# Kernel optimization log

Hardware: AMD Instinct MI355X
Metric: run time of the kernel (lower is better)

The kernel has to match this reference:

```python
import jax, jax.numpy as jnp
import numpy as np

N, C_IN, C_OUT, HID, H = 4096, 512, 512, 128, 4
HEAD_OUT = C_OUT // H  # 128
MID = 4 * C_OUT        # 2048
R = 1.0                # spatial radius r
L = 48                 # sequence window l
NEG = -1e9


def layer_norm(x, g, b, eps=1e-5):
    m = jnp.mean(x, axis=-1, keepdims=True)
    v = jnp.mean(jnp.square(x - m), axis=-1, keepdims=True)
    return (x - m) * jax.lax.rsqrt(v + eps) * g + b


def setup_inputs() -> dict:
    key = jax.random.key(0)
    ks = jax.random.split(key, 16)
    s = lambda fan: 1.0 / np.sqrt(fan)
    return {
        "x":   jax.random.normal(ks[0], (N, C_IN), jnp.float32),
        "pos": jax.random.normal(ks[1], (N, 3), jnp.float32),
        "ori": jax.random.normal(ks[2], (N, 3), jnp.float32),
        "seq": jnp.arange(N, dtype=jnp.int64) if jax.config.jax_enable_x64 else jnp.arange(N, dtype=jnp.int32),
        "batch": jnp.sort(jax.random.randint(ks[3], (N,), 0, 8)),
        "ln1_g": jnp.ones((C_IN,), jnp.float32),
        "ln1_b": jnp.zeros((C_IN,), jnp.float32),
        "ln2_g": jnp.ones((C_OUT,), jnp.float32),
        "ln2_b": jnp.zeros((C_OUT,), jnp.float32),
        "Wq": jax.random.normal(ks[4], (H, C_IN, HID), jnp.float32) * s(C_IN),
        "Wk": jax.random.normal(ks[5], (H, C_IN, HID), jnp.float32) * s(C_IN),
        "Wv": jax.random.normal(ks[6], (H, C_IN, HID), jnp.float32) * s(C_IN),
        "Wo": jax.random.normal(ks[7], (H, HID, HEAD_OUT), jnp.float32) * s(HID),
        "lnm_g": jnp.ones((MID,), jnp.float32),
        "lnm_b": jnp.zeros((MID,), jnp.float32),
        "W1": jax.random.normal(ks[8], (C_OUT, MID), jnp.float32) * s(C_OUT),
        "W2": jax.random.normal(ks[9], (MID, C_OUT), jnp.float32) * s(MID),
    }


def _block(x, pos, ori, seq, batch, ln1_g, ln1_b, ln2_g, ln2_b,
           Wq, Wk, Wv, Wo, lnm_g, lnm_b, W1, W2):
    identity = x
    xn = layer_norm(x, ln1_g, ln1_b)

    # geometry/sequence neighborhood mask: same graph, ||dp||<=r, |ds|<=l
    d2 = jnp.sum(jnp.square(pos[:, None, :] - pos[None, :, :]), axis=-1)  # [N,N]
    ds = jnp.abs(seq[:, None] - seq[None, :])
    mask = (batch[:, None] == batch[None, :]) & (d2 <= R * R) & (ds <= L)

    # all heads at once (original loops over heads; math identical)
    q = jnp.einsum('nc,hcd->hnd', xn, Wq)
    k = jnp.einsum('nc,hcd->hnd', xn, Wk)
    v = jnp.einsum('nc,hcd->hnd', xn, Wv)
    gbias = ori @ ori.T  # geometric orientation bias [N,N]
    scores = jnp.einsum('hnd,hmd->hnm', q, k) / np.sqrt(HID) + gbias[None]
    scores = jnp.where(mask[None], scores, NEG)
    attn = jax.nn.softmax(scores, axis=-1)
    o = jnp.einsum('hnm,hmd->hnd', attn, v)
    o = jnp.einsum('hnd,hde->hne', o, Wo)               # [H,N,HEAD_OUT]
    o = jnp.transpose(o, (1, 0, 2)).reshape(N, C_OUT)   # concat heads

    x = o + identity
    identity = x
    h = layer_norm(x, ln2_g, ln2_b) @ W1
    h = jax.nn.relu(layer_norm(h, lnm_g, lnm_b))
    return h @ W2 + identity


def reference(x, pos, ori, seq, batch, ln1_g, ln1_b, ln2_g, ln2_b,
              Wq, Wk, Wv, Wo, lnm_g, lnm_b, W1, W2):
    return _block(x, pos, ori, seq, batch, ln1_g, ln1_b, ln2_g, ln2_b,
                  Wq, Wk, Wv, Wo, lnm_g, lnm_b, W1, W2)
```

## Files before the change

kernel.cpp:

```cpp
#include <hip/hip_runtime.h>

typedef unsigned short u16;
typedef unsigned int u32;
typedef float f32x4 __attribute__((ext_vector_type(4)));
typedef __bf16 bf16x8 __attribute__((ext_vector_type(8)));

#define N_TOK 4096
#define QKV_LD 1536
#define NH 4
#define HID 128
#define C_OUT 512

__device__ __forceinline__ float b2f(u16 u) { return __uint_as_float(((u32)u) << 16); }
__device__ __forceinline__ u16 f2b(float f) {
  u32 u = __float_as_uint(f);
  u32 r = (u + 0x7fffu + ((u >> 16) & 1u)) >> 16;
  return (u16)r;
}

__global__ __launch_bounds__(256) void transpose_tile(
    const float* __restrict__ src, u16* __restrict__ dst, int R, int C)
{
  __shared__ u16 tile[32][33];
  const int b = blockIdx.z;
  const int c0 = blockIdx.x * 32, r0 = blockIdx.y * 32;
  const int tx = threadIdx.x & 31, ty = threadIdx.x >> 5;
  const float* s = src + (size_t)b * R * C;
  u16* d = dst + (size_t)b * R * C;
#pragma unroll
  for (int i = 0; i < 32; i += 8)
    tile[ty + i][tx] = f2b(s[(size_t)(r0 + ty + i) * C + c0 + tx]);
  __syncthreads();
#pragma unroll
  for (int i = 0; i < 32; i += 8)
    d[(size_t)(c0 + ty + i) * R + r0 + tx] = tile[tx][ty + i];
}

__global__ __launch_bounds__(256) void transpose_qkv(
    const float* __restrict__ Wq, const float* __restrict__ Wk,
    const float* __restrict__ Wv, u16* __restrict__ dst)
{
  __shared__ u16 tile[32][33];
  const int z = blockIdx.z;
  const int which = z >> 2, b = z & 3;
  const float* src = (which == 0) ? Wq : (which == 1) ? Wk : Wv;
  const int R = 512, C = 128;
  const int c0 = blockIdx.x * 32, r0 = blockIdx.y * 32;
  const int tx = threadIdx.x & 31, ty = threadIdx.x >> 5;
  const float* s = src + (size_t)b * R * C;
  u16* d = dst + (size_t)which * 4 * R * C + (size_t)b * R * C;
#pragma unroll
  for (int i = 0; i < 32; i += 8)
    tile[ty + i][tx] = f2b(s[(size_t)(r0 + ty + i) * C + c0 + tx]);
  __syncthreads();
#pragma unroll
  for (int i = 0; i < 32; i += 8)
    d[(size_t)(c0 + ty + i) * R + r0 + tx] = tile[tx][ty + i];
}

__global__ __launch_bounds__(256) void ln_kernel(
    const void* __restrict__ x, const float* __restrict__ g,
    const float* __restrict__ b, u16* __restrict__ y,
    int C, int in_f32, int do_relu)
{
  int row = blockIdx.x;
  int tid = threadIdx.x;
  const float* xf = (const float*)x + (size_t)row * C;
  const u16* xh = (const u16*)x + (size_t)row * C;
  float s1 = 0.f, s2 = 0.f;
  for (int c = tid * 4; c < C; c += 1024) {
    float4 v;
    if (in_f32) v = *(const float4*)(xf + c);
    else {
      uint2 u = *(const uint2*)(xh + c);
      v.x = b2f((u16)u.x); v.y = b2f((u16)(u.x >> 16));
      v.z = b2f((u16)u.y); v.w = b2f((u16)(u.y >> 16));
    }
    s1 += v.x + v.y + v.z + v.w;
    s2 += v.x * v.x + v.y * v.y + v.z * v.z + v.w * v.w;
  }
  __shared__ float red[2][4];
  for (int o = 32; o; o >>= 1) { s1 += __shfl_down(s1, o); s2 += __shfl_down(s2, o); }
  int lane = tid & 63, w = tid >> 6;
  if (lane == 0) { red[0][w] = s1; red[1][w] = s2; }
  __syncthreads();
  s1 = red[0][0] + red[0][1] + red[0][2] + red[0][3];
  s2 = red[1][0] + red[1][1] + red[1][2] + red[1][3];
  float mean = s1 / C;
  float var = s2 / C - mean * mean;
  float rs = rsqrtf(fmaxf(var, 0.f) + 1e-5f);
  u16* yr = y + (size_t)row * C;
  for (int c = tid * 4; c < C; c += 1024) {
    float4 v;
    if (in_f32) v = *(const float4*)(xf + c);
    else {
      uint2 u = *(const uint2*)(xh + c);
      v.x = b2f((u16)u.x); v.y = b2f((u16)(u.x >> 16));
      v.z = b2f((u16)u.y); v.w = b2f((u16)(u.y >> 16));
    }
    float4 gg = *(const float4*)(g + c);
    float4 bb = *(const float4*)(b + c);
    float o0 = (v.x - mean) * rs * gg.x + bb.x;
    float o1 = (v.y - mean) * rs * gg.y + bb.y;
    float o2 = (v.z - mean) * rs * gg.z + bb.z;
    float o3 = (v.w - mean) * rs * gg.w + bb.w;
    if (do_relu) {
      o0 = fmaxf(o0, 0.f); o1 = fmaxf(o1, 0.f);
      o2 = fmaxf(o2, 0.f); o3 = fmaxf(o3, 0.f);
    }
    u16 t[4] = {f2b(o0), f2b(o1), f2b(o2), f2b(o3)};
    *(uint2*)(yr + c) = *(const uint2*)t;
  }
}

#define LDK 40
__global__ __launch_bounds__(512, 4) void gemm128(
    const u16* __restrict__ A, int lda,
    const u16* __restrict__ Bt,
    void* __restrict__ C, int ldc, int outf32,
    const float* __restrict__ res,
    int Kslice, int Ktot, int bd, int atomic)
{
  __shared__ u16 As[128 * LDK];
  __shared__ u16 Bs[128 * LDK];
  const int bn = blockIdx.x, bm = blockIdx.y;
  const int m0 = bm * 128, n0 = bn * 128;
  const int kbase = blockIdx.z * Kslice;
  const int abase = (bd ? bn * Ktot : 0) + kbase;
  const int tid = threadIdx.x;
  const int lane = tid & 63, w = tid >> 6;
  const int wm = (w & 1) * 64;
  const int wn = (w >> 1) * 32;
  const int l16 = lane & 15, quad = lane >> 4;

  const int sr = tid >> 2, sc = (tid & 3) * 8;
  const u16* PA = A + (size_t)(m0 + sr) * lda + abase + sc;
  const u16* PB = Bt + (size_t)(n0 + sr) * Ktot + kbase + sc;

  f32x4 acc[4][2];
#pragma unroll
  for (int i = 0; i < 4; i++)
#pragma unroll
    for (int j = 0; j < 2; j++) acc[i][j] = (f32x4){0.f, 0.f, 0.f, 0.f};

  int4 pa = *(const int4*)PA;
  int4 pb = *(const int4*)PB;
  for (int kk = 0; kk < Kslice; kk += 32) {
    *(int4*)&As[sr * LDK + sc] = pa;
    *(int4*)&Bs[sr * LDK + sc] = pb;
    __syncthreads();
    if (kk + 32 < Kslice) {
      PA += 32; pa = *(const int4*)PA;
      PB += 32; pb = *(const int4*)PB;
    }
    bf16x8 af[4], bfr[2];
#pragma unroll
    for (int mt = 0; mt < 4; mt++)
      af[mt] = *(const bf16x8*)&As[(wm + mt * 16 + l16) * LDK + quad * 8];
#pragma unroll
    for (int nt = 0; nt < 2; nt++)
      bfr[nt] = *(const bf16x8*)&Bs[(wn + nt * 16 + l16) * LDK + quad * 8];
#pragma unroll
    for (int mt = 0; mt < 4; mt++)
#pragma unroll
      for (int nt = 0; nt < 2; nt++)
        acc[mt][nt] = __builtin_amdgcn_mfma_f32_16x16x32_bf16(
            af[mt], bfr[nt], acc[mt][nt], 0, 0, 0);
    __syncthreads();
  }

#pragma unroll
  for (int mt = 0; mt < 4; mt++)
#pragma unroll
    for (int nt = 0; nt < 2; nt++)
#pragma unroll
      for (int r = 0; r < 4; r++) {
        int gr = m0 + wm + mt * 16 + quad * 4 + r;
        int gc = n0 + wn + nt * 16 + l16;
        size_t off = (size_t)gr * ldc + gc;
        float v = acc[mt][nt][r];
        if (atomic) {
          atomicAdd((float*)C + off, v);
        } else {
          if (res) v += res[off];
          if (outf32) ((float*)C)[off] = v;
          else        ((u16*)C)[off] = f2b(v);
        }
      }
}

#define TQ 16
#define BAND 112
#define KROW 136
#define PROW 120
__global__ __launch_bounds__(256) void attn_mfma(
    const u16* __restrict__ qkv, const float* __restrict__ pos,
    const float* __restrict__ ori, const int* __restrict__ batch,
    const u16* __restrict__ wot, const float* __restrict__ xres,
    float* __restrict__ out)
{
  const int h = blockIdx.y;
  const int i0 = blockIdx.x * TQ;
  const int j0 = i0 - 48;
  const int tid = threadIdx.x;
  const int lane = tid & 63, w = tid >> 6;
  const int l16 = lane & 15, quad = lane >> 4;

  __shared__ u16 kv[128 * KROW];
  __shared__ u16 qp[TQ * KROW];
  __shared__ float ps[TQ * PROW];
  __shared__ float bpx[BAND], bpy[BAND], bpz[BAND];
  __shared__ float box_[BAND], boy_[BAND], boz_[BAND];
  __shared__ int bb[BAND];

  for (int t = tid; t < BAND; t += 256) {
    int j = j0 + t;
    if (j >= 0 && j < N_TOK) {
      bpx[t] = pos[j * 3 + 0]; bpy[t] = pos[j * 3 + 1]; bpz[t] = pos[j * 3 + 2];
      box_[t] = ori[j * 3 + 0]; boy_[t] = ori[j * 3 + 1]; boz_[t] = ori[j * 3 + 2];
      bb[t] = batch[j];
    } else {
      bpx[t] = bpy[t] = bpz[t] = 0.f;
      box_[t] = boy_[t] = boz_[t] = 0.f;
      bb[t] = -12345;
    }
  }
  for (int idx = tid; idx < BAND * 16; idx += 256) {
    int t = idx >> 4, c8 = (idx & 15) * 8;
    int j = j0 + t;
    int4 val = {0, 0, 0, 0};
    if (j >= 0 && j < N_TOK)
      val = *(const int4*)&qkv[(size_t)j * QKV_LD + 512 + h * HID + c8];
    *(int4*)&kv[t * KROW + c8] = val;
  }
  {
    int q = tid >> 4, c8 = (tid & 15) * 8;
    *(int4*)&qp[q * KROW + c8] =
        *(const int4*)&qkv[(size_t)(i0 + q) * QKV_LD + h * HID + c8];
  }
  __syncthreads();

  {
    bf16x8 af[4];
#pragma unroll
    for (int kc = 0; kc < 4; kc++)
      af[kc] = *(const bf16x8*)&qp[l16 * KROW + kc * 32 + quad * 8];
#pragma unroll
    for (int ti = 0; ti < 2; ti++) {
      int tt = w + ti * 4;
      if (tt < 7) {
        f32x4 acc = (f32x4){0.f, 0.f, 0.f, 0.f};
#pragma unroll
        for (int kc = 0; kc < 4; kc++) {
          bf16x8 bf = *(const bf16x8*)&kv[(tt * 16 + l16) * KROW + kc * 32 + quad * 8];
          acc = __builtin_amdgcn_mfma_f32_16x16x32_bf16(af[kc], bf, acc, 0, 0, 0);
        }
        int t = tt * 16 + l16;
#pragma unroll
        for (int r = 0; r < 4; r++) {
          int q = quad * 4 + r, iq = q + 48;
          int dseq = iq - t;
          bool ok = (bb[t] == bb[iq]) && (dseq <= 48) && (dseq >= -48);
          {
#pragma clang fp contract(off)
            float dx = bpx[iq] - bpx[t], dy = bpy[iq] - bpy[t], dz = bpz[iq] - bpz[t];
            float d2 = dx * dx + dy * dy + dz * dz;
            ok = ok && (d2 <= 1.0f);
          }
          float s = -1e9f;
          if (ok) {
            float gb = box_[iq] * box_[t] + boy_[iq] * boy_[t] + boz_[iq] * boz_[t];
            s = acc[r] * 0.08838834764831845f + gb;
          }
          ps[q * PROW + t] = s;
        }
      }
    }
  }
  __syncthreads();

  for (int idx = tid; idx < BAND * 32; idx += 256) {
    int t = idx >> 5, d4 = (idx & 31) * 4;
    int j = j0 + t;
    uint2 val; val.x = 0; val.y = 0;
    if (j >= 0 && j < N_TOK)
      val = *(const uint2*)&qkv[(size_t)j * QKV_LD + 1024 + h * HID + d4];
    u16 e[4] = {(u16)val.x, (u16)(val.x >> 16), (u16)val.y, (u16)(val.y >> 16)};
#pragma unroll
    for (int jj = 0; jj < 4; jj++) {
      int dd = (jj + tid) & 3;
      kv[(d4 + dd) * KROW + t] = e[dd];
    }
  }
  for (int idx = tid; idx < 128 * 16; idx += 256) {
    int d = idx >> 4, t = BAND + (idx & 15);
    kv[d * KROW + t] = 0;
  }
  {
    int row = tid >> 4, sub = tid & 15;
    float vals[7];
    float m = -1e30f;
#pragma unroll
    for (int i = 0; i < 7; i++) {
      vals[i] = ps[row * PROW + sub + i * 16];
      m = fmaxf(m, vals[i]);
    }
#pragma unroll
    for (int o = 8; o; o >>= 1) m = fmaxf(m, __shfl_xor(m, o));
    float s = 0.f;
#pragma unroll
    for (int i = 0; i < 7; i++) { vals[i] = __expf(vals[i] - m); s += vals[i]; }
#pragma unroll
    for (int o = 8; o; o >>= 1) s += __shfl_xor(s, o);
    float inv = 1.f / s;
#pragma unroll
    for (int i = 0; i < 7; i++)
      qp[row * KROW + sub + i * 16] = f2b(vals[i] * inv);
    qp[row * KROW + BAND + sub] = 0;
  }
  __syncthreads();

  u16 obuf[2][4];
  {
    bf16x8 paf[4];
#pragma unroll
    for (int kc = 0; kc < 4; kc++)
      paf[kc] = *(const bf16x8*)&qp[l16 * KROW + kc * 32 + quad * 8];
#pragma unroll
    for (int ti = 0; ti < 2; ti++) {
      int dt = w + ti * 4;
      f32x4 acc = (f32x4){0.f, 0.f, 0.f, 0.f};
#pragma unroll
      for (int kc = 0; kc < 4; kc++) {
        bf16x8 bf = *(const bf16x8*)&kv[(dt * 16 + l16) * KROW + kc * 32 + quad * 8];
        acc = __builtin_amdgcn_mfma_f32_16x16x32_bf16(paf[kc], bf, acc, 0, 0, 0);
      }
#pragma unroll
      for (int r = 0; r < 4; r++) obuf[ti][r] = f2b(acc[r]);
    }
  }
  __syncthreads();

#pragma unroll
  for (int ti = 0; ti < 2; ti++) {
    int dt = w + ti * 4;
#pragma unroll
    for (int r = 0; r < 4; r++)
      qp[(quad * 4 + r) * KROW + dt * 16 + l16] = obuf[ti][r];
  }
  {
    const u16* wsrc = wot + (size_t)h * HID * HID;
    for (int idx = tid; idx < 128 * 16; idx += 256) {
      int e = idx >> 4, c8 = (idx & 15) * 8;
      *(int4*)&kv[e * KROW + c8] = *(const int4*)&wsrc[e * HID + c8];
    }
  }
  __syncthreads();

  {
    bf16x8 oaf[4];
#pragma unroll
    for (int kc = 0; kc < 4; kc++)
      oaf[kc] = *(const bf16x8*)&qp[l16 * KROW + kc * 32 + quad * 8];
#pragma unroll
    for (int ti = 0; ti < 2; ti++) {
      int et = w + ti * 4;
      f32x4 acc = (f32x4){0.f, 0.f, 0.f, 0.f};
#pragma unroll
      for (int kc = 0; kc < 4; kc++) {
        bf16x8 bf = *(const bf16x8*)&kv[(et * 16 + l16) * KROW + kc * 32 + quad * 8];
        acc = __builtin_amdgcn_mfma_f32_16x16x32_bf16(oaf[kc], bf, acc, 0, 0, 0);
      }
#pragma unroll
      for (int r = 0; r < 4; r++) {
        int q = quad * 4 + r;
        size_t off = (size_t)(i0 + q) * C_OUT + h * HID + et * 16 + l16;
        out[off] = acc[r] + xres[off];
      }
    }
  }
}

#define MB (1048576)
extern "C" void kernel_launch(void* const* d_in, const int* in_sizes, int n_in,
                              void* d_out, int out_size, void* d_ws, size_t ws_size,
                              hipStream_t stream) {
  const float* x    = (const float*)d_in[0];
  const float* pos  = (const float*)d_in[1];
  const float* ori  = (const float*)d_in[2];
  const int*   batch = (const int*)d_in[4];
  const float* ln1g = (const float*)d_in[5];
  const float* ln1b = (const float*)d_in[6];
  const float* ln2g = (const float*)d_in[7];
  const float* ln2b = (const float*)d_in[8];
  const float* Wq = (const float*)d_in[9];
  const float* Wk = (const float*)d_in[10];
  const float* Wv = (const float*)d_in[11];
  const float* Wo = (const float*)d_in[12];
  const float* lnmg = (const float*)d_in[13];
  const float* lnmb = (const float*)d_in[14];
  const float* W1 = (const float*)d_in[15];
  const float* W2 = (const float*)d_in[16];
  float* out = (float*)d_out;

  char* ws = (char*)d_ws;
  u16* xn    = (u16*)(ws + 0);
  u16* x1n   = (u16*)(ws + 0);
  u16* qkv   = (u16*)(ws + 4 * MB);
  u16* h     = (u16*)(ws + 4 * MB);
  u16* Wot   = (u16*)(ws + 16 * MB);
  u16* Btqkv = (u16*)(ws + 20 * MB);
  u16* W2t   = (u16*)(ws + 20 * MB);
  u16* W1t   = (u16*)(ws + 22 * MB);

  transpose_qkv<<<dim3(4, 16, 12), 256, 0, stream>>>(Wq, Wk, Wv, Btqkv);
  transpose_tile<<<dim3(64, 16, 1), 256, 0, stream>>>(W1, W1t, 512, 2048);

  ln_kernel<<<dim3(4096), 256, 0, stream>>>(x, ln1g, ln1b, xn, 512, 1, 0);
  gemm128<<<dim3(12, 32, 1), 512, 0, stream>>>(xn, 512, Btqkv, qkv, QKV_LD, 0,
                                               nullptr, 512, 512, 0, 0);
  transpose_tile<<<dim3(16, 64, 1), 256, 0, stream>>>(W2, W2t, 2048, 512);
  transpose_tile<<<dim3(4, 4, 4), 256, 0, stream>>>(Wo, Wot, 128, 128);

  attn_mfma<<<dim3(256, NH), 256, 0, stream>>>(qkv, pos, ori, batch, Wot, x, out);

  ln_kernel<<<dim3(4096), 256, 0, stream>>>(out, ln2g, ln2b, x1n, 512, 1, 0);
  gemm128<<<dim3(16, 32, 1), 512, 0, stream>>>(x1n, 512, W1t, h, 2048, 0,
                                               nullptr, 512, 512, 0, 0);
  ln_kernel<<<dim3(4096), 256, 0, stream>>>(h, lnmg, lnmb, h, 2048, 0, 1);
  gemm128<<<dim3(4, 32, 4), 512, 0, stream>>>(h, 2048, W2t, out, 512, 1,
                                              nullptr, 512, 2048, 0, 1);
}
```

Baseline: 221.6 us.

## Merge weight transposes, specialize layernorm kernels, swizzle attention blocks, halve split-K

Folds the QKV, W1 and Wo weight transposes into one launch, cutting launch count. Replaces the generic layernorm with specialized kernels: a one-wave-per-row 512-wide f32 version with no shared memory, and a 2048-wide bf16+ReLU version with a single load pass. Remaps attention block indices into a strided order and reduces the W2 GEMM split-K from 4 to 2, which means fewer atomic adds per output but fewer blocks to fill the GPU.

Measured after the change: 200.5 us. 9.6% less time.

```diff
diff --git a/kernel.cpp b/kernel.cpp
--- a/kernel.cpp
+++ b/kernel.cpp
@@ -36,19 +36,36 @@
     d[(size_t)(c0 + ty + i) * R + r0 + tx] = tile[tx][ty + i];
 }
 
-__global__ __launch_bounds__(256) void transpose_qkv(
+__global__ __launch_bounds__(256) void transpose_all(
     const float* __restrict__ Wq, const float* __restrict__ Wk,
-    const float* __restrict__ Wv, u16* __restrict__ dst)
+    const float* __restrict__ Wv, const float* __restrict__ Wo,
+    const float* __restrict__ W1,
+    u16* __restrict__ Btqkv, u16* __restrict__ Wot, u16* __restrict__ W1t)
 {
   __shared__ u16 tile[32][33];
-  const int z = blockIdx.z;
-  const int which = z >> 2, b = z & 3;
-  const float* src = (which == 0) ? Wq : (which == 1) ? Wk : Wv;
-  const int R = 512, C = 128;
-  const int c0 = blockIdx.x * 32, r0 = blockIdx.y * 32;
+  const int idx = blockIdx.x;
+  const float* s; u16* d; int R, C, r0, c0;
+  if (idx < 1024) {
+    s = W1; d = W1t; R = 512; C = 2048;
+    r0 = (idx >> 6) * 32; c0 = (idx & 63) * 32;
+  } else if (idx < 1792) {
+    int i = idx - 1024;
+    int z = i >> 6, rem = i & 63;
+    int which = z >> 2, b = z & 3;
+    const float* base = (which == 0) ? Wq : (which == 1) ? Wk : Wv;
+    s = base + (size_t)b * 512 * 128;
+    d = Btqkv + (size_t)which * 4 * 512 * 128 + (size_t)b * 512 * 128;
+    R = 512; C = 128;
+    r0 = (rem >> 2) * 32; c0 = (rem & 3) * 32;
+  } else {
+    int i = idx - 1792;
+    int b = i >> 4, rem = i & 15;
+    s = Wo + (size_t)b * 128 * 128;
+    d = Wot + (size_t)b * 128 * 128;
+    R = 128; C = 128;
+    r0 = (rem >> 2) * 32; c0 = (rem & 3) * 32;
+  }
   const int tx = threadIdx.x & 31, ty = threadIdx.x >> 5;
-  const float* s = src + (size_t)b * R * C;
-  u16* d = dst + (size_t)which * 4 * R * C + (size_t)b * R * C;
 #pragma unroll
   for (int i = 0; i < 32; i += 8)
     tile[ty + i][tx] = f2b(s[(size_t)(r0 + ty + i) * C + c0 + tx]);
@@ -58,59 +75,70 @@
     d[(size_t)(c0 + ty + i) * R + r0 + tx] = tile[tx][ty + i];
 }
 
-__global__ __launch_bounds__(256) void ln_kernel(
-    const void* __restrict__ x, const float* __restrict__ g,
-    const float* __restrict__ b, u16* __restrict__ y,
-    int C, int in_f32, int do_relu)
-{
-  int row = blockIdx.x;
-  int tid = threadIdx.x;
-  const float* xf = (const float*)x + (size_t)row * C;
-  const u16* xh = (const u16*)x + (size_t)row * C;
+__global__ __launch_bounds__(256) void ln512_f32(
+    const float* __restrict__ x, const float* __restrict__ g,
+    const float* __restrict__ b, u16* __restrict__ y)
+{
+  const int lane = threadIdx.x & 63;
+  const int row = blockIdx.x * 4 + (threadIdx.x >> 6);
+  const float* xr = x + (size_t)row * 512;
+  const int c = lane * 8;
+  float4 a0 = *(const float4*)(xr + c);
+  float4 a1 = *(const float4*)(xr + c + 4);
+  float v[8] = {a0.x, a0.y, a0.z, a0.w, a1.x, a1.y, a1.z, a1.w};
   float s1 = 0.f, s2 = 0.f;
-  for (int c = tid * 4; c < C; c += 1024) {
-    float4 v;
-    if (in_f32) v = *(const float4*)(xf + c);
-    else {
-      uint2 u = *(const uint2*)(xh + c);
-      v.x = b2f((u16)u.x); v.y = b2f((u16)(u.x >> 16));
-      v.z = b2f((u16)u.y); v.w = b2f((u16)(u.y >> 16));
-    }
-    s1 += v.x + v.y + v.z + v.w;
-    s2 += v.x * v.x + v.y * v.y + v.z * v.z + v.w * v.w;
-  }
+#pragma unroll
+  for (int i = 0; i < 8; i++) { s1 += v[i]; s2 += v[i] * v[i]; }
+#pragma unroll
+  for (int o = 32; o; o >>= 1) { s1 += __shfl_xor(s1, o); s2 += __shfl_xor(s2, o); }
+  float mean = s1 * (1.f / 512.f);
+  float var = s2 * (1.f / 512.f) - mean * mean;
+  float rs = rsqrtf(fmaxf(var, 0.f) + 1e-5f);
+  float4 g0 = *(const float4*)(g + c), g1 = *(const float4*)(g + c + 4);
+  float4 b0 = *(const float4*)(b + c), b1 = *(const float4*)(b + c + 4);
+  float gg[8] = {g0.x, g0.y, g0.z, g0.w, g1.x, g1.y, g1.z, g1.w};
+  float bb[8] = {b0.x, b0.y, b0.z, b0.w, b1.x, b1.y, b1.z, b1.w};
+  u16 t[8];
+#pragma unroll
+  for (int i = 0; i < 8; i++) t[i] = f2b((v[i] - mean) * rs * gg[i] + bb[i]);
+  *(uint4*)(y + (size_t)row * 512 + c) = *(const uint4*)t;
+}
+
+__global__ __launch_bounds__(256) void ln2048_bf16_relu(
+    const u16* __restrict__ x, const float* __restrict__ g,
+    const float* __restrict__ b, u16* __restrict__ y)
+{
+  const int row = blockIdx.x, tid = threadIdx.x;
+  const int c = tid * 8;
+  const u16* xr = x + (size_t)row * 2048;
+  uint4 u = *(const uint4*)(xr + c);
+  u16 e[8]; *(uint4*)e = u;
+  float v[8];
+#pragma unroll
+  for (int i = 0; i < 8; i++) v[i] = b2f(e[i]);
+  float s1 = 0.f, s2 = 0.f;
+#pragma unroll
+  for (int i = 0; i < 8; i++) { s1 += v[i]; s2 += v[i] * v[i]; }
+#pragma unroll
+  for (int o = 32; o; o >>= 1) { s1 += __shfl_xor(s1, o); s2 += __shfl_xor(s2, o); }
   __shared__ float red[2][4];
-  for (int o = 32; o; o >>= 1) { s1 += __shfl_down(s1, o); s2 += __shfl_down(s2, o); }
   int lane = tid & 63, w = tid >> 6;
   if (lane == 0) { red[0][w] = s1; red[1][w] = s2; }
   __syncthreads();
   s1 = red[0][0] + red[0][1] + red[0][2] + red[0][3];
   s2 = red[1][0] + red[1][1] + red[1][2] + red[1][3];
-  float mean = s1 / C;
-  float var = s2 / C - mean * mean;
+  float mean = s1 * (1.f / 2048.f);
+  float var = s2 * (1.f / 2048.f) - mean * mean;
   float rs = rsqrtf(fmaxf(var, 0.f) + 1e-5f);
-  u16* yr = y + (size_t)row * C;
-  for (int c = tid * 4; c < C; c += 1024) {
-    float4 v;
-    if (in_f32) v = *(const float4*)(xf + c);
-    else {
-      uint2 u = *(const uint2*)(xh + c);
-      v.x = b2f((u16)u.x); v.y = b2f((u16)(u.x >> 16));
-      v.z = b2f((u16)u.y); v.w = b2f((u16)(u.y >> 16));
-    }
-    float4 gg = *(const float4*)(g + c);
-    float4 bb = *(const float4*)(b + c);
-    float o0 = (v.x - mean) * rs * gg.x + bb.x;
-    float o1 = (v.y - mean) * rs * gg.y + bb.y;
-    float o2 = (v.z - mean) * rs * gg.z + bb.z;
-    float o3 = (v.w - mean) * rs * gg.w + bb.w;
-    if (do_relu) {
-      o0 = fmaxf(o0, 0.f); o1 = fmaxf(o1, 0.f);
-      o2 = fmaxf(o2, 0.f); o3 = fmaxf(o3, 0.f);
-    }
-    u16 t[4] = {f2b(o0), f2b(o1), f2b(o2), f2b(o3)};
-    *(uint2*)(yr + c) = *(const uint2*)t;
-  }
+  float4 g0 = *(const float4*)(g + c), g1 = *(const float4*)(g + c + 4);
+  float4 b0 = *(const float4*)(b + c), b1 = *(const float4*)(b + c + 4);
+  float gg[8] = {g0.x, g0.y, g0.z, g0.w, g1.x, g1.y, g1.z, g1.w};
+  float bb[8] = {b0.x, b0.y, b0.z, b0.w, b1.x, b1.y, b1.z, b1.w};
+  u16 t[8];
+#pragma unroll
+  for (int i = 0; i < 8; i++)
+    t[i] = f2b(fmaxf((v[i] - mean) * rs * gg[i] + bb[i], 0.f));
+  *(uint4*)(y + (size_t)row * 2048 + c) = *(const uint4*)t;
 }
 
 #define LDK 40
@@ -200,7 +228,8 @@
     float* __restrict__ out)
 {
   const int h = blockIdx.y;
-  const int i0 = blockIdx.x * TQ;
+  const int bxs = (blockIdx.x & 7) * 32 + (blockIdx.x >> 3);
+  const int i0 = bxs * TQ;
   const int j0 = i0 - 48;
   const int tid = threadIdx.x;
   const int lane = tid & 63, w = tid >> 6;
@@ -413,21 +442,17 @@
   u16* W2t   = (u16*)(ws + 20 * MB);
   u16* W1t   = (u16*)(ws + 22 * MB);
 
-  transpose_qkv<<<dim3(4, 16, 12), 256, 0, stream>>>(Wq, Wk, Wv, Btqkv);
-  transpose_tile<<<dim3(64, 16, 1), 256, 0, stream>>>(W1, W1t, 512, 2048);
-
-  ln_kernel<<<dim3(4096), 256, 0, stream>>>(x, ln1g, ln1b, xn, 512, 1, 0);
+  transpose_all<<<dim3(1856), 256, 0, stream>>>(Wq, Wk, Wv, Wo, W1,
+                                                Btqkv, Wot, W1t);
+  ln512_f32<<<dim3(1024), 256, 0, stream>>>(x, ln1g, ln1b, xn);
   gemm128<<<dim3(12, 32, 1), 512, 0, stream>>>(xn, 512, Btqkv, qkv, QKV_LD, 0,
                                                nullptr, 512, 512, 0, 0);
   transpose_tile<<<dim3(16, 64, 1), 256, 0, stream>>>(W2, W2t, 2048, 512);
-  transpose_tile<<<dim3(4, 4, 4), 256, 0, stream>>>(Wo, Wot, 128, 128);
-
   attn_mfma<<<dim3(256, NH), 256, 0, stream>>>(qkv, pos, ori, batch, Wot, x, out);
-
-  ln_kernel<<<dim3(4096), 256, 0, stream>>>(out, ln2g, ln2b, x1n, 512, 1, 0);
+  ln512_f32<<<dim3(1024), 256, 0, stream>>>(out, ln2g, ln2b, x1n);
   gemm128<<<dim3(16, 32, 1), 512, 0, stream>>>(x1n, 512, W1t, h, 2048, 0,
                                                nullptr, 512, 512, 0, 0);
-  ln_kernel<<<dim3(4096), 256, 0, stream>>>(h, lnmg, lnmb, h, 2048, 0, 1);
-  gemm128<<<dim3(4, 32, 4), 512, 0, stream>>>(h, 2048, W2t, out, 512, 1,
-                                              nullptr, 512, 2048, 0, 1);
-}
+  ln2048_bf16_relu<<<dim3(4096), 256, 0, stream>>>(h, lnmg, lnmb, h);
+  gemm128<<<dim3(4, 32, 2), 512, 0, stream>>>(h, 2048, W2t, out, 512, 1,
+                                              nullptr, 1024, 2048, 0, 1);
+}
```
